# Kernel tuning notes

Hardware: AMD Instinct MI355X
Metric: run time of the kernel (lower is better)

Reference implementation:

```python
import jax, jax.numpy as jnp
import numpy as np

DIM = 128
N_HEADS = 8

def setup_inputs() -> dict:
    key = jax.random.key(0)
    k1, k2, k3 = jax.random.split(key, 3)
    B, N = 8, 1024
    inner = DIM * N_HEADS  # 1024
    x = jax.random.normal(k1, (B, N, DIM), dtype=jnp.float32)
    w_qkv = jax.random.normal(k2, (DIM, inner * 3), dtype=jnp.float32) * (DIM ** -0.5)
    w_out = jax.random.normal(k3, (inner, DIM), dtype=jnp.float32) * (inner ** -0.5)
    b_out = jnp.zeros((DIM,), dtype=jnp.float32)
    return {"x": x, "w_qkv": w_qkv, "w_out": w_out, "b_out": b_out}

def reference(x, w_qkv, w_out, b_out):
    B, N, _ = x.shape
    h, d = N_HEADS, DIM  # per-head dim = dim (module's convention)
    qkv = x @ w_qkv                       # [B, N, 3*h*d]
    q, k, v = jnp.split(qkv, 3, axis=-1)  # each [B, N, h*d]
    to_heads = lambda t: t.reshape(B, N, h, d).transpose(0, 2, 1, 3)  # b h n d
    q, k, v = to_heads(q), to_heads(k), to_heads(v)
    scores = jnp.einsum('bhid,bhjd->bhij', q, k) * (d ** -0.5)
    A = jax.nn.softmax(scores, axis=-1)
    z = jnp.einsum('bhij,bhjd->bhid', A, v)
    z = z.transpose(0, 2, 1, 3).reshape(B, N, h * d)  # b n (h d)
    # to_out: Dense(dim) + Dropout (inference => identity)
    return z @ w_out + b_out
```

## Files before the change

### kernel.cpp

```cpp
#include <hip/hip_runtime.h>

#define BATCH 8
#define SEQ   1024
#define DIM   128
#define HEADS 8
#define NQKV  3072
#define QSZ   (BATCH*HEADS*SEQ*DIM)

typedef __attribute__((ext_vector_type(4))) float floatx4;
typedef __attribute__((ext_vector_type(8))) __bf16 bf16x8;

__device__ __forceinline__ unsigned short bf16bits(float f) {
  union { float f; unsigned int u; } v;
  v.f = f;
  unsigned int u = v.u;
  u += 0x7fffu + ((u >> 16) & 1u);
  return (unsigned short)(u >> 16);
}

#define XBSZ  (BATCH*SEQ*DIM)
#define WQTSZ (NQKV*DIM)

__global__ __launch_bounds__(256, 2)
void prep1_kernel(const float* __restrict__ x, const float* __restrict__ wqkv,
                  unsigned short* __restrict__ ws) {
  unsigned short* xb  = ws + (size_t)3 * QSZ;
  unsigned short* wqt = xb + XBSZ;
  const int blk = blockIdx.x, t = threadIdx.x;
  if (blk < 512) {
    size_t base = (size_t)blk * 2048 + t * 8;
    float4 f0 = *(const float4*)(x + base);
    float4 f1 = *(const float4*)(x + base + 4);
    ushort4 a, b;
    a.x = bf16bits(f0.x); a.y = bf16bits(f0.y); a.z = bf16bits(f0.z); a.w = bf16bits(f0.w);
    b.x = bf16bits(f1.x); b.y = bf16bits(f1.y); b.z = bf16bits(f1.z); b.w = bf16bits(f1.w);
    *(ushort4*)(xb + base)     = a;
    *(ushort4*)(xb + base + 4) = b;
  } else {
    __shared__ __align__(16) unsigned short L[64 * 136];
    const int n0 = (blk - 512) * 64;
    const int n = t & 63, kg = t >> 6;
    for (int i = 0; i < 32; ++i) {
      int k = kg * 32 + i;
      L[n * 136 + k] = bf16bits(wqkv[(size_t)k * NQKV + n0 + n]);
    }
    __syncthreads();
    for (int i = 0; i < 4; ++i) {
      int cid = i * 256 + t;
      int r = cid >> 4, ch = cid & 15;
      *(bf16x8*)(wqt + (size_t)(n0 + r) * 128 + ch * 8) = *(const bf16x8*)&L[r * 136 + ch * 8];
    }
  }
}

__global__ __launch_bounds__(256, 2)
void prep2_kernel(const float* __restrict__ wout, unsigned short* __restrict__ ws) {
  __shared__ __align__(16) unsigned short L[128 * 136];
  const int k0 = blockIdx.x * 128, t = threadIdx.x;
  const int n = t & 127, kg = t >> 7;
  for (int i = 0; i < 64; ++i) {
    int k = kg * 64 + i;
    L[n * 136 + k] = bf16bits(wout[(size_t)(k0 + k) * DIM + n]);
  }
  __syncthreads();
  for (int i = 0; i < 8; ++i) {
    int cid = i * 256 + t;
    int r = cid >> 4, ch = cid & 15;
    *(bf16x8*)(ws + (size_t)r * 1024 + k0 + ch * 8) = *(const bf16x8*)&L[r * 136 + ch * 8];
  }
}

__global__ __launch_bounds__(256, 2)
void qkv_kernel(unsigned short* __restrict__ ws) {
  const unsigned short* xb  = ws + (size_t)3 * QSZ;
  const unsigned short* wqt = xb + XBSZ;

  const int tn = blockIdx.x % 24;
  const int tm = blockIdx.x / 24;
  const int m0 = tm * 128, n0 = tn * 128;

  __shared__ __align__(16) unsigned short As[128 * 136];
  __shared__ __align__(16) unsigned short Bt[128 * 136];

  const int t = threadIdx.x;
  const int lane = t & 63, wv = t >> 6;
  const int l16 = lane & 15, qd = lane >> 4;

  for (int i = 0; i < 8; ++i) {
    int cid = i * 256 + t;
    int r = cid >> 4, ch = cid & 15;
    *(bf16x8*)&As[r * 136 + ch * 8] = *(const bf16x8*)(xb + (size_t)(m0 + r) * 128 + ch * 8);
    *(bf16x8*)&Bt[r * 136 + ch * 8] = *(const bf16x8*)(wqt + (size_t)(n0 + r) * 128 + ch * 8);
  }
  __syncthreads();

  const int mo = (wv >> 1) * 64, no = (wv & 1) * 64;
  floatx4 acc[4][4] = {};
  for (int k0 = 0; k0 < 128; k0 += 32) {
    bf16x8 af[4], bfv[4];
    for (int mt = 0; mt < 4; ++mt)
      af[mt] = *(const bf16x8*)&As[(mo + mt * 16 + l16) * 136 + k0 + qd * 8];
    for (int nt = 0; nt < 4; ++nt)
      bfv[nt] = *(const bf16x8*)&Bt[(no + nt * 16 + l16) * 136 + k0 + qd * 8];
    for (int mt = 0; mt < 4; ++mt)
      for (int nt = 0; nt < 4; ++nt)
        acc[mt][nt] = __builtin_amdgcn_mfma_f32_16x16x32_bf16(af[mt], bfv[nt], acc[mt][nt], 0, 0, 0);
  }

  const int s = tn >> 3;
  const int h = tn & 7;
  const float scale = (s == 0) ? 0.08838834764831845f : 1.0f;

  __syncthreads();
  unsigned short* Cs = As;
  if (s < 2) {
    for (int mt = 0; mt < 4; ++mt)
      for (int nt = 0; nt < 4; ++nt)
        for (int r = 0; r < 4; ++r)
          Cs[(mo + mt * 16 + qd * 4 + r) * 136 + no + nt * 16 + l16] =
              bf16bits(acc[mt][nt][r] * scale);
  } else {
    for (int mt = 0; mt < 4; ++mt)
      for (int nt = 0; nt < 4; ++nt)
        for (int r = 0; r < 4; ++r)
          Cs[(no + nt * 16 + l16) * 136 + mo + mt * 16 + qd * 4 + r] =
              bf16bits(acc[mt][nt][r]);
  }
  __syncthreads();

  const int b = m0 >> 10, nseq0 = m0 & 1023;
  const int bh = b * HEADS + h;
  if (s < 2) {
    unsigned short* dst = ws + (size_t)s * QSZ + ((size_t)bh * SEQ + nseq0) * 128;
    for (int i = 0; i < 8; ++i) {
      int cid = i * 256 + t;
      int mr = cid >> 4, ch = cid & 15;
      *(bf16x8*)(dst + (size_t)mr * 128 + ch * 8) = *(const bf16x8*)&Cs[mr * 136 + ch * 8];
    }
  } else {
    unsigned short* dst = ws + (size_t)2 * QSZ + (size_t)bh * DIM * SEQ + nseq0;
    for (int i = 0; i < 8; ++i) {
      int cid = i * 256 + t;
      int cr = cid >> 4, ch = cid & 15;
      *(bf16x8*)(dst + (size_t)cr * SEQ + ch * 8) = *(const bf16x8*)&Cs[cr * 136 + ch * 8];
    }
  }
}

__global__ __launch_bounds__(256, 3)
void attn_kernel(unsigned short* __restrict__ ws) {
  const unsigned short* Q  = ws;
  const unsigned short* K  = ws + (size_t)QSZ;
  const unsigned short* VT = ws + (size_t)2 * QSZ;
  unsigned short*       Z  = ws + (size_t)3 * QSZ;

  const int bh = blockIdx.x & 63;
  const int qt = blockIdx.x >> 6;
  const int t = threadIdx.x, lane = t & 63, wv = t >> 6;
  const int l16 = lane & 15, qd = lane >> 4;

  __shared__ __align__(16) unsigned short Ks[64 * 136];
  __shared__ __align__(16) unsigned short Vs[128 * 72];
  __shared__ __align__(16) unsigned short Pw[4][32 * 72];

  const size_t qbase = ((size_t)bh * SEQ + qt * 128 + wv * 32) * DIM;
  bf16x8 qf[2][4];
  for (int mt = 0; mt < 2; ++mt)
    for (int ks = 0; ks < 4; ++ks)
      qf[mt][ks] = *(const bf16x8*)(Q + qbase + (size_t)(mt * 16 + l16) * DIM + ks * 32 + qd * 8);

  int kkey[4], kd0[4], vd[4], vkk[4];
  for (int i = 0; i < 4; ++i) {
    int linear = i * 2048 + t * 8;
    kkey[i] = linear >> 7; kd0[i] = linear & 127;
    vd[i]   = linear >> 6; vkk[i] = linear & 63;
  }
  const unsigned short* Kb = K  + (size_t)bh * SEQ * DIM;
  const unsigned short* Vb = VT + (size_t)bh * DIM * SEQ;

  bf16x8 kreg[4], vreg[4];
  auto fetch = [&](int kb) {
    for (int i = 0; i < 4; ++i) {
      kreg[i] = *(const bf16x8*)(Kb + (size_t)(kb + kkey[i]) * DIM + kd0[i]);
      vreg[i] = *(const bf16x8*)(Vb + (size_t)vd[i] * SEQ + kb + vkk[i]);
    }
  };
  fetch(0);

  floatx4 o[2][8] = {};
  float lsum[2][4] = {};
  unsigned short* pw = Pw[wv];

  for (int kt = 0; kt < 16; ++kt) {
    __syncthreads();
    for (int i = 0; i < 4; ++i) {
      *(bf16x8*)&Ks[kkey[i] * 136 + kd0[i]] = kreg[i];
      *(bf16x8*)&Vs[vd[i] * 72 + vkk[i]]    = vreg[i];
    }
    __syncthreads();
    if (kt < 15) fetch((kt + 1) * 64);

    floatx4 s[2][4] = {};
    for (int ks = 0; ks < 4; ++ks) {
      bf16x8 kf[4];
      for (int nt = 0; nt < 4; ++nt)
        kf[nt] = *(const bf16x8*)&Ks[(nt * 16 + l16) * 136 + ks * 32 + qd * 8];
      for (int mt = 0; mt < 2; ++mt)
        for (int nt = 0; nt < 4; ++nt)
          s[mt][nt] = __builtin_amdgcn_mfma_f32_16x16x32_bf16(qf[mt][ks], kf[nt], s[mt][nt], 0, 0, 0);
    }

    for (int mt = 0; mt < 2; ++mt)
      for (int nt = 0; nt < 4; ++nt)
        for (int r = 0; r < 4; ++r) {
          float p = __expf(s[mt][nt][r] - 10.0f);
          lsum[mt][r] += p;
          pw[(mt * 16 + qd * 4 + r) * 72 + nt * 16 + l16] = bf16bits(p);
        }

    for (int ks2 = 0; ks2 < 2; ++ks2) {
      bf16x8 pf[2];
      for (int mt = 0; mt < 2; ++mt)
        pf[mt] = *(const bf16x8*)&pw[(mt * 16 + l16) * 72 + ks2 * 32 + qd * 8];
      for (int nt = 0; nt < 8; ++nt) {
        bf16x8 vf = *(const bf16x8*)&Vs[(nt * 16 + l16) * 72 + ks2 * 32 + qd * 8];
        for (int mt = 0; mt < 2; ++mt)
          o[mt][nt] = __builtin_amdgcn_mfma_f32_16x16x32_bf16(pf[mt], vf, o[mt][nt], 0, 0, 0);
      }
    }
  }

  const int b = bh >> 3, h = bh & 7;
  for (int mt = 0; mt < 2; ++mt)
    for (int r = 0; r < 4; ++r) {
      float l = lsum[mt][r];
      for (int off = 1; off < 16; off <<= 1)
        l += __shfl_xor(l, off, 64);
      float inv = 1.f / l;
      int n = qt * 128 + wv * 32 + mt * 16 + qd * 4 + r;
      size_t rowoff = ((size_t)b * SEQ + n) * (HEADS * DIM) + h * DIM;
      for (int nt = 0; nt < 8; ++nt)
        Z[rowoff + nt * 16 + l16] = bf16bits(o[mt][nt][r] * inv);
    }
}

__global__ __launch_bounds__(256, 2)
void out_kernel(const unsigned short* __restrict__ ws, const float* __restrict__ bias,
                float* __restrict__ out) {
  const unsigned short* Z   = ws + (size_t)3 * QSZ;
  const unsigned short* wot = ws;
  const int m0 = blockIdx.x * 32;
  __shared__ __align__(16) unsigned short As[32 * 136];
  __shared__ __align__(16) unsigned short Bt[128 * 136];

  const int t = threadIdx.x, lane = t & 63, wv = t >> 6;
  const int l16 = lane & 15, qd = lane >> 4;
  const int rg = (wv & 1) * 16, cg = (wv >> 1) * 64;

  int ar[2], ac[2], br[8], bc[8];
  for (int i = 0; i < 2; ++i) { int cid = i * 256 + t; ar[i] = cid >> 4; ac[i] = cid & 15; }
  for (int i = 0; i < 8; ++i) { int cid = i * 256 + t; br[i] = cid >> 4; bc[i] = cid & 15; }

  bf16x8 areg[2], breg[8];
  auto fetch = [&](int k0) {
    for (int i = 0; i < 2; ++i)
      areg[i] = *(const bf16x8*)(Z + (size_t)(m0 + ar[i]) * 1024 + k0 + ac[i] * 8);
    for (int i = 0; i < 8; ++i)
      breg[i] = *(const bf16x8*)(wot + (size_t)br[i] * 1024 + k0 + bc[i] * 8);
  };
  fetch(0);

  floatx4 acc[4] = {};
  for (int k0 = 0; k0 < 1024; k0 += 128) {
    __syncthreads();
    for (int i = 0; i < 2; ++i) *(bf16x8*)&As[ar[i] * 136 + ac[i] * 8] = areg[i];
    for (int i = 0; i < 8; ++i) *(bf16x8*)&Bt[br[i] * 136 + bc[i] * 8] = breg[i];
    __syncthreads();
    if (k0 < 896) fetch(k0 + 128);

    for (int ks = 0; ks < 4; ++ks) {
      bf16x8 af = *(const bf16x8*)&As[(rg + l16) * 136 + ks * 32 + qd * 8];
      for (int nt = 0; nt < 4; ++nt) {
        bf16x8 bfv = *(const bf16x8*)&Bt[(cg + nt * 16 + l16) * 136 + ks * 32 + qd * 8];
        acc[nt] = __builtin_amdgcn_mfma_f32_16x16x32_bf16(af, bfv, acc[nt], 0, 0, 0);
      }
    }
  }

  for (int nt = 0; nt < 4; ++nt)
    for (int r = 0; r < 4; ++r) {
      int row = m0 + rg + qd * 4 + r;
      int col = cg + nt * 16 + l16;
      out[(size_t)row * DIM + col] = acc[nt][r] + bias[col];
    }
}

extern "C" void kernel_launch(void* const* d_in, const int* in_sizes, int n_in,
                              void* d_out, int out_size, void* d_ws, size_t ws_size,
                              hipStream_t stream) {
  (void)in_sizes; (void)n_in; (void)out_size; (void)ws_size;
  const float* x     = (const float*)d_in[0];
  const float* w_qkv = (const float*)d_in[1];
  const float* w_out = (const float*)d_in[2];
  const float* b_out = (const float*)d_in[3];
  float* out = (float*)d_out;
  unsigned short* ws = (unsigned short*)d_ws;

  prep1_kernel<<<dim3(560), dim3(256), 0, stream>>>(x, w_qkv, ws);
  qkv_kernel<<<dim3(64 * 24), dim3(256), 0, stream>>>(ws);
  attn_kernel<<<dim3(64 * 8), dim3(256), 0, stream>>>(ws);
  prep2_kernel<<<dim3(8), dim3(256), 0, stream>>>(w_out, ws);
  out_kernel<<<dim3(256), dim3(256), 0, stream>>>(ws, b_out, out);
}
```

Measured before the change: 164.0 us.

## Read MFMA operands directly from global memory and stage attention output via LDS

The QKV GEMM now loads MFMA fragments straight from global memory instead of staging tiles in shared memory, and its occupancy hint is raised. Attention drops the shared-memory V tile and reads V^T fragments directly from global per key block. It also writes Z through an LDS buffer so global stores are 16-byte vectors. The output GEMM is rewritten as a register-only kernel with 16-row tiles and twice the blocks. These changes trade LDS traffic and barriers for more uncoalesced or redundant global and L2 reads, and they change occupancy hints.

```diff
diff --git a/kernel.cpp b/kernel.cpp
--- a/kernel.cpp
+++ b/kernel.cpp
@@ -70,7 +70,7 @@
   }
 }
 
-__global__ __launch_bounds__(256, 2)
+__global__ __launch_bounds__(256, 3)
 void qkv_kernel(unsigned short* __restrict__ ws) {
   const unsigned short* xb  = ws + (size_t)3 * QSZ;
   const unsigned short* wqt = xb + XBSZ;
@@ -79,29 +79,20 @@
   const int tm = blockIdx.x / 24;
   const int m0 = tm * 128, n0 = tn * 128;
 
-  __shared__ __align__(16) unsigned short As[128 * 136];
-  __shared__ __align__(16) unsigned short Bt[128 * 136];
+  __shared__ __align__(16) unsigned short Cs[128 * 136];
 
   const int t = threadIdx.x;
   const int lane = t & 63, wv = t >> 6;
   const int l16 = lane & 15, qd = lane >> 4;
-
-  for (int i = 0; i < 8; ++i) {
-    int cid = i * 256 + t;
-    int r = cid >> 4, ch = cid & 15;
-    *(bf16x8*)&As[r * 136 + ch * 8] = *(const bf16x8*)(xb + (size_t)(m0 + r) * 128 + ch * 8);
-    *(bf16x8*)&Bt[r * 136 + ch * 8] = *(const bf16x8*)(wqt + (size_t)(n0 + r) * 128 + ch * 8);
-  }
-  __syncthreads();
-
   const int mo = (wv >> 1) * 64, no = (wv & 1) * 64;
+
   floatx4 acc[4][4] = {};
-  for (int k0 = 0; k0 < 128; k0 += 32) {
+  for (int ks = 0; ks < 4; ++ks) {
     bf16x8 af[4], bfv[4];
     for (int mt = 0; mt < 4; ++mt)
-      af[mt] = *(const bf16x8*)&As[(mo + mt * 16 + l16) * 136 + k0 + qd * 8];
+      af[mt] = *(const bf16x8*)(xb + (size_t)(m0 + mo + mt * 16 + l16) * 128 + ks * 32 + qd * 8);
     for (int nt = 0; nt < 4; ++nt)
-      bfv[nt] = *(const bf16x8*)&Bt[(no + nt * 16 + l16) * 136 + k0 + qd * 8];
+      bfv[nt] = *(const bf16x8*)(wqt + (size_t)(n0 + no + nt * 16 + l16) * 128 + ks * 32 + qd * 8);
     for (int mt = 0; mt < 4; ++mt)
       for (int nt = 0; nt < 4; ++nt)
         acc[mt][nt] = __builtin_amdgcn_mfma_f32_16x16x32_bf16(af[mt], bfv[nt], acc[mt][nt], 0, 0, 0);
@@ -111,8 +102,6 @@
   const int h = tn & 7;
   const float scale = (s == 0) ? 0.08838834764831845f : 1.0f;
 
-  __syncthreads();
-  unsigned short* Cs = As;
   if (s < 2) {
     for (int mt = 0; mt < 4; ++mt)
       for (int nt = 0; nt < 4; ++nt)
@@ -147,7 +136,7 @@
   }
 }
 
-__global__ __launch_bounds__(256, 3)
+__global__ __launch_bounds__(256, 2)
 void attn_kernel(unsigned short* __restrict__ ws) {
   const unsigned short* Q  = ws;
   const unsigned short* K  = ws + (size_t)QSZ;
@@ -159,9 +148,9 @@
   const int t = threadIdx.x, lane = t & 63, wv = t >> 6;
   const int l16 = lane & 15, qd = lane >> 4;
 
-  __shared__ __align__(16) unsigned short Ks[64 * 136];
-  __shared__ __align__(16) unsigned short Vs[128 * 72];
-  __shared__ __align__(16) unsigned short Pw[4][32 * 72];
+  __shared__ __align__(16) unsigned short smem[17920];
+  unsigned short* Ks = smem;
+  unsigned short* pw = smem + 8704 + wv * 2304;
 
   const size_t qbase = ((size_t)bh * SEQ + qt * 128 + wv * 32) * DIM;
   bf16x8 qf[2][4];
@@ -169,36 +158,31 @@
     for (int ks = 0; ks < 4; ++ks)
       qf[mt][ks] = *(const bf16x8*)(Q + qbase + (size_t)(mt * 16 + l16) * DIM + ks * 32 + qd * 8);
 
-  int kkey[4], kd0[4], vd[4], vkk[4];
+  int kkey[4], kd0[4];
   for (int i = 0; i < 4; ++i) {
     int linear = i * 2048 + t * 8;
     kkey[i] = linear >> 7; kd0[i] = linear & 127;
-    vd[i]   = linear >> 6; vkk[i] = linear & 63;
   }
   const unsigned short* Kb = K  + (size_t)bh * SEQ * DIM;
   const unsigned short* Vb = VT + (size_t)bh * DIM * SEQ;
 
-  bf16x8 kreg[4], vreg[4];
+  bf16x8 kreg[4];
   auto fetch = [&](int kb) {
-    for (int i = 0; i < 4; ++i) {
+    for (int i = 0; i < 4; ++i)
       kreg[i] = *(const bf16x8*)(Kb + (size_t)(kb + kkey[i]) * DIM + kd0[i]);
-      vreg[i] = *(const bf16x8*)(Vb + (size_t)vd[i] * SEQ + kb + vkk[i]);
-    }
   };
   fetch(0);
 
   floatx4 o[2][8] = {};
   float lsum[2][4] = {};
-  unsigned short* pw = Pw[wv];
 
   for (int kt = 0; kt < 16; ++kt) {
+    const int kb = kt * 64;
     __syncthreads();
-    for (int i = 0; i < 4; ++i) {
+    for (int i = 0; i < 4; ++i)
       *(bf16x8*)&Ks[kkey[i] * 136 + kd0[i]] = kreg[i];
-      *(bf16x8*)&Vs[vd[i] * 72 + vkk[i]]    = vreg[i];
-    }
     __syncthreads();
-    if (kt < 15) fetch((kt + 1) * 64);
+    if (kt < 15) fetch(kb + 64);
 
     floatx4 s[2][4] = {};
     for (int ks = 0; ks < 4; ++ks) {
@@ -209,6 +193,10 @@
         for (int nt = 0; nt < 4; ++nt)
           s[mt][nt] = __builtin_amdgcn_mfma_f32_16x16x32_bf16(qf[mt][ks], kf[nt], s[mt][nt], 0, 0, 0);
     }
+
+    bf16x8 vf[8];
+    for (int nt = 0; nt < 8; ++nt)
+      vf[nt] = *(const bf16x8*)(Vb + (size_t)(nt * 16 + l16) * SEQ + kb + qd * 8);
 
     for (int mt = 0; mt < 2; ++mt)
       for (int nt = 0; nt < 4; ++nt)
@@ -218,81 +206,75 @@
           pw[(mt * 16 + qd * 4 + r) * 72 + nt * 16 + l16] = bf16bits(p);
         }
 
-    for (int ks2 = 0; ks2 < 2; ++ks2) {
+    {
       bf16x8 pf[2];
       for (int mt = 0; mt < 2; ++mt)
-        pf[mt] = *(const bf16x8*)&pw[(mt * 16 + l16) * 72 + ks2 * 32 + qd * 8];
-      for (int nt = 0; nt < 8; ++nt) {
-        bf16x8 vf = *(const bf16x8*)&Vs[(nt * 16 + l16) * 72 + ks2 * 32 + qd * 8];
+        pf[mt] = *(const bf16x8*)&pw[(mt * 16 + l16) * 72 + qd * 8];
+      for (int nt = 0; nt < 8; ++nt)
         for (int mt = 0; mt < 2; ++mt)
-          o[mt][nt] = __builtin_amdgcn_mfma_f32_16x16x32_bf16(pf[mt], vf, o[mt][nt], 0, 0, 0);
-      }
-    }
-  }
-
-  const int b = bh >> 3, h = bh & 7;
+          o[mt][nt] = __builtin_amdgcn_mfma_f32_16x16x32_bf16(pf[mt], vf[nt], o[mt][nt], 0, 0, 0);
+    }
+    for (int nt = 0; nt < 8; ++nt)
+      vf[nt] = *(const bf16x8*)(Vb + (size_t)(nt * 16 + l16) * SEQ + kb + 32 + qd * 8);
+    {
+      bf16x8 pf[2];
+      for (int mt = 0; mt < 2; ++mt)
+        pf[mt] = *(const bf16x8*)&pw[(mt * 16 + l16) * 72 + 32 + qd * 8];
+      for (int nt = 0; nt < 8; ++nt)
+        for (int mt = 0; mt < 2; ++mt)
+          o[mt][nt] = __builtin_amdgcn_mfma_f32_16x16x32_bf16(pf[mt], vf[nt], o[mt][nt], 0, 0, 0);
+    }
+  }
+
+  __syncthreads();
+  unsigned short* zb = smem + wv * 4352;
   for (int mt = 0; mt < 2; ++mt)
     for (int r = 0; r < 4; ++r) {
       float l = lsum[mt][r];
       for (int off = 1; off < 16; off <<= 1)
         l += __shfl_xor(l, off, 64);
       float inv = 1.f / l;
-      int n = qt * 128 + wv * 32 + mt * 16 + qd * 4 + r;
-      size_t rowoff = ((size_t)b * SEQ + n) * (HEADS * DIM) + h * DIM;
+      int row = mt * 16 + qd * 4 + r;
       for (int nt = 0; nt < 8; ++nt)
-        Z[rowoff + nt * 16 + l16] = bf16bits(o[mt][nt][r] * inv);
-    }
-}
-
-__global__ __launch_bounds__(256, 2)
+        zb[row * 136 + nt * 16 + l16] = bf16bits(o[mt][nt][r] * inv);
+    }
+  const int b = bh >> 3, h = bh & 7;
+  for (int i = 0; i < 8; ++i) {
+    int c = i * 64 + lane;
+    int row = c >> 4, ch = c & 15;
+    int n = qt * 128 + wv * 32 + row;
+    size_t off = ((size_t)b * SEQ + n) * (HEADS * DIM) + h * DIM + ch * 8;
+    *(bf16x8*)(Z + off) = *(const bf16x8*)&zb[row * 136 + ch * 8];
+  }
+}
+
+__global__ __launch_bounds__(256, 4)
 void out_kernel(const unsigned short* __restrict__ ws, const float* __restrict__ bias,
                 float* __restrict__ out) {
   const unsigned short* Z   = ws + (size_t)3 * QSZ;
   const unsigned short* wot = ws;
-  const int m0 = blockIdx.x * 32;
-  __shared__ __align__(16) unsigned short As[32 * 136];
-  __shared__ __align__(16) unsigned short Bt[128 * 136];
-
+  const int m0 = blockIdx.x * 16;
   const int t = threadIdx.x, lane = t & 63, wv = t >> 6;
   const int l16 = lane & 15, qd = lane >> 4;
-  const int rg = (wv & 1) * 16, cg = (wv >> 1) * 64;
-
-  int ar[2], ac[2], br[8], bc[8];
-  for (int i = 0; i < 2; ++i) { int cid = i * 256 + t; ar[i] = cid >> 4; ac[i] = cid & 15; }
-  for (int i = 0; i < 8; ++i) { int cid = i * 256 + t; br[i] = cid >> 4; bc[i] = cid & 15; }
-
-  bf16x8 areg[2], breg[8];
-  auto fetch = [&](int k0) {
-    for (int i = 0; i < 2; ++i)
-      areg[i] = *(const bf16x8*)(Z + (size_t)(m0 + ar[i]) * 1024 + k0 + ac[i] * 8);
-    for (int i = 0; i < 8; ++i)
-      breg[i] = *(const bf16x8*)(wot + (size_t)br[i] * 1024 + k0 + bc[i] * 8);
-  };
-  fetch(0);
-
-  floatx4 acc[4] = {};
-  for (int k0 = 0; k0 < 1024; k0 += 128) {
-    __syncthreads();
-    for (int i = 0; i < 2; ++i) *(bf16x8*)&As[ar[i] * 136 + ac[i] * 8] = areg[i];
-    for (int i = 0; i < 8; ++i) *(bf16x8*)&Bt[br[i] * 136 + bc[i] * 8] = breg[i];
-    __syncthreads();
-    if (k0 < 896) fetch(k0 + 128);
-
-    for (int ks = 0; ks < 4; ++ks) {
-      bf16x8 af = *(const bf16x8*)&As[(rg + l16) * 136 + ks * 32 + qd * 8];
-      for (int nt = 0; nt < 4; ++nt) {
-        bf16x8 bfv = *(const bf16x8*)&Bt[(cg + nt * 16 + l16) * 136 + ks * 32 + qd * 8];
-        acc[nt] = __builtin_amdgcn_mfma_f32_16x16x32_bf16(af, bfv, acc[nt], 0, 0, 0);
-      }
-    }
-  }
-
-  for (int nt = 0; nt < 4; ++nt)
+  const int cg = wv * 32;
+
+  floatx4 acc[2] = {};
+  for (int kc = 0; kc < 1024; kc += 32) {
+    bf16x8 af = *(const bf16x8*)(Z + (size_t)(m0 + l16) * 1024 + kc + qd * 8);
+    for (int nt = 0; nt < 2; ++nt) {
+      bf16x8 bfv = *(const bf16x8*)(wot + (size_t)(cg + nt * 16 + l16) * 1024 + kc + qd * 8);
+      acc[nt] = __builtin_amdgcn_mfma_f32_16x16x32_bf16(af, bfv, acc[nt], 0, 0, 0);
+    }
+  }
+
+  for (int nt = 0; nt < 2; ++nt) {
+    int col = cg + nt * 16 + l16;
+    float bv = bias[col];
     for (int r = 0; r < 4; ++r) {
-      int row = m0 + rg + qd * 4 + r;
-      int col = cg + nt * 16 + l16;
-      out[(size_t)row * DIM + col] = acc[nt][r] + bias[col];
-    }
+      int row = m0 + qd * 4 + r;
+      out[(size_t)row * DIM + col] = acc[nt][r] + bv;
+    }
+  }
 }
 
 extern "C" void kernel_launch(void* const* d_in, const int* in_sizes, int n_in,
@@ -310,5 +292,5 @@
   qkv_kernel<<<dim3(64 * 24), dim3(256), 0, stream>>>(ws);
   attn_kernel<<<dim3(64 * 8), dim3(256), 0, stream>>>(ws);
   prep2_kernel<<<dim3(8), dim3(256), 0, stream>>>(w_out, ws);
-  out_kernel<<<dim3(256), dim3(256), 0, stream>>>(ws, b_out, out);
-}
+  out_kernel<<<dim3(512), dim3(256), 0, stream>>>(ws, b_out, out);
+}
```

New measurement: 199.2 us. 1.21x slower.
